# Kernel tuning notes

Measured on AMD Instinct MI355X. Metric: run time of the kernel, lower is better.

Reference implementation:

```python
import jax, jax.numpy as jnp
import numpy as np

B, N, NNZ = 8, 1024, 1_048_576
F_IN, F_OUT = 64, 64
EPS = 1e-10


def mlp(x, W1, b1, W2, b2):
    # Linear-ReLU-Linear-ReLU, matches nn.Sequential in the torch module
    h = jax.nn.relu(x @ W1 + b1)
    return jax.nn.relu(h @ W2 + b2)


def setup_inputs() -> dict:
    key = jax.random.key(0)
    ks = jax.random.split(key, 16)
    s1 = 1.0 / np.sqrt(F_IN)
    s2 = 1.0 / np.sqrt(F_OUT)
    return {
        "x": jax.random.normal(ks[0], (B, N, F_IN), dtype=jnp.float32),
        "W_val": jax.random.normal(ks[1], (NNZ, F_OUT), dtype=jnp.float32),
        "e_b": jax.random.randint(ks[2], (NNZ,), 0, B, dtype=jnp.int32),
        "e_i": jax.random.randint(ks[3], (NNZ,), 0, N, dtype=jnp.int32),
        "e_j": jax.random.randint(ks[4], (NNZ,), 0, N, dtype=jnp.int32),
        "e_k": jax.random.randint(ks[5], (NNZ,), 0, N, dtype=jnp.int32),
        # n_func_3 params
        "W1": jax.random.normal(ks[6], (F_IN, F_OUT), dtype=jnp.float32) * s1,
        "b1": jnp.zeros((F_OUT,), dtype=jnp.float32),
        "W2": jax.random.normal(ks[7], (F_OUT, F_OUT), dtype=jnp.float32) * s2,
        "b2": jnp.zeros((F_OUT,), dtype=jnp.float32),
        # n_self_func params
        "Ws1": jax.random.normal(ks[8], (F_IN, F_OUT), dtype=jnp.float32) * s1,
        "bs1": jnp.zeros((F_OUT,), dtype=jnp.float32),
        "Ws2": jax.random.normal(ks[9], (F_OUT, F_OUT), dtype=jnp.float32) * s2,
        "bs2": jnp.zeros((F_OUT,), dtype=jnp.float32),
    }


def reference(x, W_val, e_b, e_i, e_j, e_k, W1, b1, W2, b2, Ws1, bs1, Ws2, bs2):
    # --- forward_sparse, order=3, norm=True ---
    # normalization of binary A over dims (2..order) -> 1/deg(b, i)
    seg = e_b.astype(jnp.int32) * N + e_i.astype(jnp.int32)
    deg = jax.ops.segment_sum(jnp.ones((NNZ,), x.dtype), seg, num_segments=B * N)
    a_val = 1.0 / (deg[seg] + EPS)                      # [nnz]

    x1 = mlp(x, W1, b1, W2, b2)                         # [B, N, F_OUT]

    # gather node features at hyperedge tails, multiply across orders
    tp = a_val[:, None] * W_val                         # [nnz, F_OUT]
    tp = tp * x1[e_b, e_k] * x1[e_b, e_j]               # i=0 -> last index, i=1 -> index 2

    # scatter-accumulate to hyperedge head nodes (index_put_ accumulate=True)
    x_new = jnp.zeros_like(x1).at[e_b, e_i].add(tp)     # [B, N, F_OUT]

    # x2 += n_self_func(x)
    x_new = x_new + mlp(x, Ws1, bs1, Ws2, bs2)
    return x_new
```

## Files before the change

kernel.cpp:

```cpp
#include <hip/hip_runtime.h>

#define BN 8192
#define NP 1024
#define NF 64
#define NSEG 8192
#define NBIN 1024
#define CAPBIN 1184
#define OVF_MAX 4096
#define OVFS (1 << 30)

typedef float f32x4 __attribute__((ext_vector_type(4)));

__global__ __launch_bounds__(1024) void prep_kernel(
    const float* __restrict__ x,
    const float* __restrict__ W1, const float* __restrict__ b1,
    const float* __restrict__ W2, const float* __restrict__ b2,
    const float* __restrict__ Ws1, const float* __restrict__ bs1,
    const float* __restrict__ Ws2, const float* __restrict__ bs2,
    const int* __restrict__ eb, const int* __restrict__ ei,
    const int* __restrict__ ej, const int* __restrict__ ek,
    int* __restrict__ gcur, int2* __restrict__ rec,
    int* __restrict__ ovf_cnt, int4* __restrict__ ovf,
    float* __restrict__ x1, float* __restrict__ out,
    int nnz, int nsb)
{
    if ((int)blockIdx.x < nsb) {
        __shared__ int hist[NBIN];
        __shared__ int cur[NBIN];
        const int t = threadIdx.x;
        hist[t] = 0;
        __syncthreads();

        int segs[8], jks[8];
        const int base = blockIdx.x * 8192;
        #pragma unroll
        for (int q = 0; q < 2; ++q) {
            const int e0 = base + (q * 1024 + t) * 4;
            if (e0 < nnz) {
                const int4 b4 = *(const int4*)(eb + e0);
                const int4 i4 = *(const int4*)(ei + e0);
                const int4 j4 = *(const int4*)(ej + e0);
                const int4 k4 = *(const int4*)(ek + e0);
                segs[q*4+0] = b4.x * NP + i4.x;  jks[q*4+0] = (j4.x << 10) | k4.x;
                segs[q*4+1] = b4.y * NP + i4.y;  jks[q*4+1] = (j4.y << 10) | k4.y;
                segs[q*4+2] = b4.z * NP + i4.z;  jks[q*4+2] = (j4.z << 10) | k4.z;
                segs[q*4+3] = b4.w * NP + i4.w;  jks[q*4+3] = (j4.w << 10) | k4.w;
                #pragma unroll
                for (int c = 0; c < 4; ++c)
                    atomicAdd(&hist[segs[q*4+c] >> 3], 1);
            } else {
                #pragma unroll
                for (int c = 0; c < 4; ++c) segs[q*4+c] = -1;
            }
        }
        __syncthreads();

        {
            const int v = hist[t];
            int c = 0;
            if (v > 0) {
                const int r = atomicAdd(&gcur[t], v);
                if (r + v <= CAPBIN) {
                    c = t * CAPBIN + r;
                } else {
                    atomicSub(&gcur[t], v);
                    c = OVFS + atomicAdd(ovf_cnt, v);
                }
            }
            cur[t] = c;
        }
        __syncthreads();

        #pragma unroll
        for (int q = 0; q < 2; ++q) {
            #pragma unroll
            for (int c = 0; c < 4; ++c) {
                const int idx = q * 4 + c;
                if (segs[idx] >= 0) {
                    const int e = base + (q * 1024 + t) * 4 + c;
                    const int seg = segs[idx];
                    const int p = atomicAdd(&cur[seg >> 3], 1);
                    if (p < OVFS) {
                        rec[p] = make_int2(e | ((seg & 7) << 20), jks[idx]);
                    } else {
                        const int o = p - OVFS;
                        if (o < OVF_MAX) ovf[o] = make_int4(seg, e, jks[idx], 0);
                    }
                }
            }
        }
    } else {
        const int row = ((int)blockIdx.x - nsb) * 16 + ((int)threadIdx.x >> 6);
        const int t = threadIdx.x & 63;
        const float xv = x[(size_t)row * NF + t];
        float a1 = b1[t], a2 = bs1[t];
        #pragma unroll 8
        for (int c = 0; c < NF; ++c) {
            const float xc = __shfl(xv, c);
            a1 = fmaf(xc, W1[c * NF + t], a1);
            a2 = fmaf(xc, Ws1[c * NF + t], a2);
        }
        const float h1 = fmaxf(a1, 0.f), h2 = fmaxf(a2, 0.f);
        float o1 = b2[t], o2 = bs2[t];
        #pragma unroll 8
        for (int c = 0; c < NF; ++c) {
            o1 = fmaf(__shfl(h1, c), W2[c * NF + t], o1);
            o2 = fmaf(__shfl(h2, c), Ws2[c * NF + t], o2);
        }
        x1[(size_t)row * NF + t]  = fmaxf(o1, 0.f);
        out[(size_t)row * NF + t] = fmaxf(o2, 0.f);
    }
}

__global__ __launch_bounds__(512, 8) void gather_kernel(
    const f32x4* __restrict__ Wv4, const f32x4* __restrict__ x14,
    const int* __restrict__ gcur, const int2* __restrict__ rec,
    const int* __restrict__ ovf_cnt, const int4* __restrict__ ovf,
    f32x4* __restrict__ out4)
{
    __shared__ int2 srt[CAPBIN];
    __shared__ int hist[8], cur2[8], base2[8];
    const int bin = blockIdx.x;
    const int t = threadIdx.x;
    const int cnt = gcur[bin];
    if (t < 8) hist[t] = 0;
    __syncthreads();

    const int2* strip = rec + (size_t)bin * CAPBIN;
    #pragma unroll
    for (int i = 0; i < 3; ++i) {
        const int idx = i * 512 + t;
        if (idx < cnt) atomicAdd(&hist[(strip[idx].x >> 20) & 7], 1);
    }
    __syncthreads();
    if (t < 8) {
        int bsum = 0;
        for (int s = 0; s < t; ++s) bsum += hist[s];
        base2[t] = bsum; cur2[t] = bsum;
    }
    __syncthreads();
    #pragma unroll
    for (int i = 0; i < 3; ++i) {
        const int idx = i * 512 + t;
        if (idx < cnt) {
            const int2 r = strip[idx];
            srt[atomicAdd(&cur2[(r.x >> 20) & 7], 1)] = r;
        }
    }
    __syncthreads();

    const int w    = t >> 6;
    const int lane = t & 63;
    const int sub  = lane >> 4;
    const int c16  = lane & 15;
    const int seg  = bin * 8 + w;
    const int b    = seg >> 10;
    const f32x4* __restrict__ x1b = x14 + ((size_t)b << 10) * 16;
    const int cs = hist[w], bs = base2[w];
    int dtrue = cs;

    f32x4 acc = {0.f, 0.f, 0.f, 0.f};
    #pragma unroll 2
    for (int it = 0; it < cs; it += 4) {
        int idx = it + sub;
        const float m = (idx < cs) ? 1.f : 0.f;
        idx = min(idx, cs - 1);
        const int2 r = srt[bs + idx];
        const int e = r.x & 0xFFFFF;
        const int j = (r.y >> 10) & 1023, k = r.y & 1023;
        const f32x4 wv = __builtin_nontemporal_load(Wv4 + (size_t)e * 16 + c16);
        const f32x4 xj = x1b[j * 16 + c16];
        const f32x4 xk = x1b[k * 16 + c16];
        acc += (m * wv) * (xj * xk);
    }

    const int novf = min(ovf_cnt[0], OVF_MAX);
    if (novf > 0) {
        for (int o = 0; o < novf; ++o) {
            const int4 r = ovf[o];
            if (r.x == seg) {
                ++dtrue;
                const float m = (sub == 0) ? 1.f : 0.f;
                const int j = (r.z >> 10) & 1023, k = r.z & 1023;
                const f32x4 wv = Wv4[(size_t)(unsigned)r.y * 16 + c16];
                acc += (m * wv) * (x1b[j * 16 + c16] * x1b[k * 16 + c16]);
            }
        }
    }

    #pragma unroll
    for (int mm = 16; mm < 64; mm <<= 1) {
        acc.x += __shfl_xor(acc.x, mm);
        acc.y += __shfl_xor(acc.y, mm);
        acc.z += __shfl_xor(acc.z, mm);
        acc.w += __shfl_xor(acc.w, mm);
    }

    if (sub == 0) {
        const float a = 1.0f / ((float)dtrue + 1e-10f);
        f32x4 o = out4[(size_t)seg * 16 + c16];
        out4[(size_t)seg * 16 + c16] = o + a * acc;
    }
}

extern "C" void kernel_launch(void* const* d_in, const int* in_sizes, int n_in,
                              void* d_out, int out_size, void* d_ws, size_t ws_size,
                              hipStream_t stream) {
    const float* x   = (const float*)d_in[0];
    const float* Wv  = (const float*)d_in[1];
    const int*   eb  = (const int*)d_in[2];
    const int*   ei  = (const int*)d_in[3];
    const int*   ej  = (const int*)d_in[4];
    const int*   ek  = (const int*)d_in[5];
    const float* W1  = (const float*)d_in[6];
    const float* b1  = (const float*)d_in[7];
    const float* W2  = (const float*)d_in[8];
    const float* b2  = (const float*)d_in[9];
    const float* Ws1 = (const float*)d_in[10];
    const float* bs1 = (const float*)d_in[11];
    const float* Ws2 = (const float*)d_in[12];
    const float* bs2 = (const float*)d_in[13];
    float* out = (float*)d_out;
    const int nnz = in_sizes[2];

    char* ws = (char*)d_ws;
    float* x1    = (float*)ws;
    int* gcur    = (int*)(ws + (2 << 20));
    int* ovf_cnt = gcur + NBIN;
    int4* ovf    = (int4*)(ws + (2 << 20) + (64 << 10));
    int2* rec    = (int2*)(ws + (4 << 20));

    const int nsb = (nnz + 8191) / 8192;
    const int nmlp = BN / 16;

    (void)hipMemsetAsync(gcur, 0, (NBIN + 1) * sizeof(int), stream);
    prep_kernel<<<nsb + nmlp, 1024, 0, stream>>>(x, W1, b1, W2, b2, Ws1, bs1, Ws2, bs2,
                                                 eb, ei, ej, ek, gcur, rec, ovf_cnt, ovf,
                                                 x1, out, nnz, nsb);
    gather_kernel<<<NBIN, 512, 0, stream>>>((const f32x4*)Wv, (const f32x4*)x1,
                                            gcur, rec, ovf_cnt, ovf, (f32x4*)out);
}
```

Measured before the change: 116.5 us.

## Split bin records evenly across waves with per-segment accumulators instead of sorting

```diff
diff --git a/kernel.cpp b/kernel.cpp
--- a/kernel.cpp
+++ b/kernel.cpp
@@ -112,94 +112,111 @@
     }
 }
 
-__global__ __launch_bounds__(512, 8) void gather_kernel(
+__global__ __launch_bounds__(512, 4) void gather_kernel(
     const f32x4* __restrict__ Wv4, const f32x4* __restrict__ x14,
     const int* __restrict__ gcur, const int2* __restrict__ rec,
     const int* __restrict__ ovf_cnt, const int4* __restrict__ ovf,
     f32x4* __restrict__ out4)
 {
-    __shared__ int2 srt[CAPBIN];
-    __shared__ int hist[8], cur2[8], base2[8];
+    __shared__ int2 srec[CAPBIN];
+    __shared__ float part[8][8][NF];
+    __shared__ float dpart[8][8];
     const int bin = blockIdx.x;
     const int t = threadIdx.x;
     const int cnt = gcur[bin];
-    if (t < 8) hist[t] = 0;
-    __syncthreads();
 
     const int2* strip = rec + (size_t)bin * CAPBIN;
-    #pragma unroll
-    for (int i = 0; i < 3; ++i) {
-        const int idx = i * 512 + t;
-        if (idx < cnt) atomicAdd(&hist[(strip[idx].x >> 20) & 7], 1);
-    }
-    __syncthreads();
-    if (t < 8) {
-        int bsum = 0;
-        for (int s = 0; s < t; ++s) bsum += hist[s];
-        base2[t] = bsum; cur2[t] = bsum;
-    }
-    __syncthreads();
-    #pragma unroll
-    for (int i = 0; i < 3; ++i) {
-        const int idx = i * 512 + t;
-        if (idx < cnt) {
-            const int2 r = strip[idx];
-            srt[atomicAdd(&cur2[(r.x >> 20) & 7], 1)] = r;
-        }
-    }
+    for (int i = t; i < cnt; i += 512)
+        srec[i] = strip[i];
     __syncthreads();
 
     const int w    = t >> 6;
     const int lane = t & 63;
     const int sub  = lane >> 4;
     const int c16  = lane & 15;
-    const int seg  = bin * 8 + w;
-    const int b    = seg >> 10;
+    const int b    = bin >> 7;
     const f32x4* __restrict__ x1b = x14 + ((size_t)b << 10) * 16;
-    const int cs = hist[w], bs = base2[w];
-    int dtrue = cs;
-
-    f32x4 acc = {0.f, 0.f, 0.f, 0.f};
-    #pragma unroll 2
-    for (int it = 0; it < cs; it += 4) {
-        int idx = it + sub;
-        const float m = (idx < cs) ? 1.f : 0.f;
-        idx = min(idx, cs - 1);
-        const int2 r = srt[bs + idx];
-        const int e = r.x & 0xFFFFF;
+
+    const int lo = (cnt * w) >> 3;
+    const int hi = (cnt * (w + 1)) >> 3;
+
+    f32x4 acc[8];
+    float dc[8];
+    #pragma unroll
+    for (int s = 0; s < 8; ++s) { acc[s] = (f32x4){0.f,0.f,0.f,0.f}; dc[s] = 0.f; }
+
+    for (int idx = lo + sub; idx < hi; idx += 4) {
+        const int2 r = srec[idx];
+        const int e  = r.x & 0xFFFFF;
+        const int ws = (r.x >> 20) & 7;
         const int j = (r.y >> 10) & 1023, k = r.y & 1023;
         const f32x4 wv = __builtin_nontemporal_load(Wv4 + (size_t)e * 16 + c16);
         const f32x4 xj = x1b[j * 16 + c16];
         const f32x4 xk = x1b[k * 16 + c16];
-        acc += (m * wv) * (xj * xk);
+        const f32x4 v = wv * (xj * xk);
+        #pragma unroll
+        for (int s = 0; s < 8; ++s) {
+            const float p = (ws == s) ? 1.f : 0.f;
+            acc[s] += p * v;
+            dc[s]  += p;
+        }
     }
 
     const int novf = min(ovf_cnt[0], OVF_MAX);
-    if (novf > 0) {
+    if (novf > 0 && w == 0) {
         for (int o = 0; o < novf; ++o) {
             const int4 r = ovf[o];
-            if (r.x == seg) {
-                ++dtrue;
+            const int s0 = r.x - bin * 8;
+            if (s0 >= 0 && s0 < 8) {
                 const float m = (sub == 0) ? 1.f : 0.f;
                 const int j = (r.z >> 10) & 1023, k = r.z & 1023;
                 const f32x4 wv = Wv4[(size_t)(unsigned)r.y * 16 + c16];
-                acc += (m * wv) * (x1b[j * 16 + c16] * x1b[k * 16 + c16]);
+                const f32x4 v = (m * wv) * (x1b[j * 16 + c16] * x1b[k * 16 + c16]);
+                #pragma unroll
+                for (int s = 0; s < 8; ++s) {
+                    const float p = (s0 == s) ? 1.f : 0.f;
+                    acc[s] += p * v;
+                    dc[s]  += p * 0.25f;
+                }
             }
         }
     }
 
     #pragma unroll
-    for (int mm = 16; mm < 64; mm <<= 1) {
-        acc.x += __shfl_xor(acc.x, mm);
-        acc.y += __shfl_xor(acc.y, mm);
-        acc.z += __shfl_xor(acc.z, mm);
-        acc.w += __shfl_xor(acc.w, mm);
-    }
-
+    for (int s = 0; s < 8; ++s) {
+        #pragma unroll
+        for (int mm = 16; mm < 64; mm <<= 1) {
+            acc[s].x += __shfl_xor(acc[s].x, mm);
+            acc[s].y += __shfl_xor(acc[s].y, mm);
+            acc[s].z += __shfl_xor(acc[s].z, mm);
+            acc[s].w += __shfl_xor(acc[s].w, mm);
+            dc[s]    += __shfl_xor(dc[s], mm);
+        }
+    }
     if (sub == 0) {
-        const float a = 1.0f / ((float)dtrue + 1e-10f);
-        f32x4 o = out4[(size_t)seg * 16 + c16];
-        out4[(size_t)seg * 16 + c16] = o + a * acc;
+        #pragma unroll
+        for (int s = 0; s < 8; ++s)
+            *(f32x4*)&part[w][s][c16 * 4] = acc[s];
+    }
+    if (lane == 0) {
+        #pragma unroll
+        for (int s = 0; s < 8; ++s) dpart[w][s] = dc[s];
+    }
+    __syncthreads();
+
+    if (t < 128) {
+        const int s = t >> 4, cc = t & 15;
+        f32x4 sum = {0.f, 0.f, 0.f, 0.f};
+        float d = 0.f;
+        #pragma unroll
+        for (int ww = 0; ww < 8; ++ww) {
+            sum += *(const f32x4*)&part[ww][s][cc * 4];
+            d += dpart[ww][s];
+        }
+        const int seg = bin * 8 + s;
+        const float a = 1.0f / (d + 1e-10f);
+        f32x4 o = out4[(size_t)seg * 16 + cc];
+        out4[(size_t)seg * 16 + cc] = o + a * sum;
     }
 }
 
```

Result: slower. 135.4 us (+16.3%).
